# Kernel tuning notes

Measured on AMD Instinct MI355X. Metric: run time of the kernel, lower is better.

## Reference

```python
import jax, jax.numpy as jnp
import numpy as np

B, Cfi, H, W = 2, 32, 192, 192
Cfp, Cfo, NUM = 1, 2, 16
N = H * W
Ct = Cfo + Cfi + Cfi + Cfp  # 67
EPS = 1e-5


def _bn(x, g, b, m, v):
    # x: (B, C, num, N); per-channel inference batchnorm
    inv = g * jax.lax.rsqrt(v + EPS)
    return x * inv[None, :, None, None] + (b - m * inv)[None, :, None, None]


def _pconv(x, Wt):
    # 1x1 conv as channel contraction: Wt (Cout, Cin), x (B, Cin, num, N)
    return jnp.einsum('oc,bcmn->bomn', Wt, x)


def setup_inputs() -> dict:
    key = jax.random.key(0)
    ks = jax.random.split(key, 32)
    inp = {
        'If': jax.random.normal(ks[0], (B, Cfi, H, W), jnp.float32),
        'Pf': jax.random.normal(ks[1], (B, Cfp, H, W), jnp.float32),
        'Ofnum': jax.random.normal(ks[2], (B, Cfo, NUM, N), jnp.float32),
        'args': jax.random.randint(ks[3], (B, NUM, N), 0, N, jnp.int64),
    }
    def conv_w(k, co, ci):
        return jax.random.normal(k, (co, ci), jnp.float32) * (1.0 / np.sqrt(ci))
    def bn_p(k, c):
        k1, k2 = jax.random.split(k)
        return (jnp.ones((c,), jnp.float32),
                jnp.zeros((c,), jnp.float32),
                jax.random.normal(k1, (c,), jnp.float32) * 0.1,
                jax.random.uniform(k2, (c,), jnp.float32, 0.5, 1.5))
    # convXF: Ct->Cfi, Cfi->Cfi (both BN+GELU)
    inp['W1'] = conv_w(ks[4], Cfi, Ct)
    inp['g1'], inp['b1'], inp['m1'], inp['v1'] = bn_p(ks[5], Cfi)
    inp['W2'] = conv_w(ks[6], Cfi, Cfi)
    inp['g2'], inp['b2'], inp['m2'], inp['v2'] = bn_p(ks[7], Cfi)
    # convXL: Cfi->Cfi (BN+GELU), Cfi->Cfi (BN only)
    inp['W3'] = conv_w(ks[8], Cfi, Cfi)
    inp['g3'], inp['b3'], inp['m3'], inp['v3'] = bn_p(ks[9], Cfi)
    inp['W4'] = conv_w(ks[10], Cfi, Cfi)
    inp['g4'], inp['b4'], inp['m4'], inp['v4'] = bn_p(ks[11], Cfi)
    # coef: Cfi -> 3, with bias
    inp['Wc'] = conv_w(ks[12], 3, Cfi)
    inp['bc'] = jax.random.normal(ks[13], (3,), jnp.float32) * 0.01
    return inp


def reference(If, Pf, Ofnum, args,
              W1, g1, b1, m1, v1,
              W2, g2, b2, m2, v2,
              W3, g3, b3, m3, v3,
              W4, g4, b4, m4, v4,
              Wc, bc):
    gelu = lambda x: jax.nn.gelu(x, approximate=False)
    If_flat = If.reshape(B, Cfi, N)   # (B, Cfi, N)
    Pf_flat = Pf.reshape(B, Cfp, N)   # (B, Cfp, M), M == N here

    # per-batch neighbor gather along flattened spatial dim
    gath = jax.vmap(lambda f, a: f[:, a])  # (C,N),(num,N) -> (C,num,N)
    IPfnum = gath(If_flat, args)            # (B, Cfi, num, N)
    Pfnum = gath(Pf_flat, args)             # (B, Cfp, num, N)
    Ifnum = jnp.broadcast_to(If_flat[:, :, None, :], (B, Cfi, NUM, N))

    X = jnp.concatenate([Ifnum, IPfnum, Pfnum, Ofnum], axis=1)  # (B, Ct, num, N)

    h = gelu(_bn(_pconv(X, W1), g1, b1, m1, v1))
    h = gelu(_bn(_pconv(h, W2), g2, b2, m2, v2))
    l = gelu(_bn(_pconv(h, W3), g3, b3, m3, v3))
    l = _bn(_pconv(l, W4), g4, b4, m4, v4)
    XF = gelu(h + l)

    feat = _pconv(XF, Wc) + bc[None, :, None, None]  # (B, 3, num, N)
    Alpha, Beta, Omega = feat[:, 0:1], feat[:, 1:2], feat[:, 2:3]
    Omega = jax.nn.softmax(Omega, axis=2)
    dout = jnp.sum(((Alpha + 1.0) * Pfnum[:, -1:] + Beta) * Omega,
                   axis=2, keepdims=True)  # (B, 1, 1, N)
    return dout.reshape(B, 1, H, W)
```

## Files before the change

### kernel.cpp

```cpp
#include <hip/hip_runtime.h>
#include <math.h>

#define BB   2
#define CFI  32
#define NN   36864
#define NUMM 16

#define ZOFSU (BB * NN * 16)

typedef __attribute__((ext_vector_type(8))) short short8;
typedef __attribute__((ext_vector_type(4))) float f4;
typedef __attribute__((ext_vector_type(16))) float f16v;
typedef __attribute__((ext_vector_type(4))) unsigned uint4v;
typedef __attribute__((ext_vector_type(2))) unsigned u2v;

static __device__ __forceinline__ f16v mm32(short8 a, short8 b, f16v c) {
    return __builtin_amdgcn_mfma_f32_32x32x16_bf16(a, b, c, 0, 0, 0);
}

template <int CTRL>
static __device__ __forceinline__ float dpp_add(float x) {
    int y = __builtin_amdgcn_update_dpp(0, __builtin_bit_cast(int, x),
                                        CTRL, 0xf, 0xf, true);
    return x + __builtin_bit_cast(float, y);
}
template <int CTRL>
static __device__ __forceinline__ float dpp_max(float x) {
    int y = __builtin_amdgcn_update_dpp(0, __builtin_bit_cast(int, x),
                                        CTRL, 0xf, 0xf, true);
    return fmaxf(x, __builtin_bit_cast(float, y));
}

static __device__ __forceinline__ float gelu_fast(float x) {
    const float x2  = x * x;
    const float q   = fmaf(-0.10294310f, x2, -2.30211813f);
    const float e   = exp2f(q * x);
    const float r   = __builtin_amdgcn_rcpf(e + 1.0f);
    return x * r;
}

static __device__ __forceinline__ unsigned bf16_rne_bits(float x) {
    unsigned u = __builtin_bit_cast(unsigned, x);
    return u + 0x7fffu + ((u >> 16) & 1u);
}
static __device__ __forceinline__ void split_pack(float x0, float x1,
                                                  unsigned& hi, unsigned& lo) {
    unsigned r0 = bf16_rne_bits(x0);
    unsigned r1 = bf16_rne_bits(x1);
    float h0 = __builtin_bit_cast(float, r0 & 0xffff0000u);
    float h1 = __builtin_bit_cast(float, r1 & 0xffff0000u);
    hi = (r0 >> 16) | (r1 & 0xffff0000u);
    unsigned s0 = bf16_rne_bits(x0 - h0);
    unsigned s1 = bf16_rne_bits(x1 - h1);
    lo = (s0 >> 16) | (s1 & 0xffff0000u);
}

static __device__ __forceinline__ unsigned pack2(float a, float b) {
    unsigned ua = __builtin_bit_cast(unsigned, a) + 0x8000u;
    unsigned ub = __builtin_bit_cast(unsigned, b) + 0x8000u;
    return (ua >> 16) | (ub & 0xffff0000u);
}
static __device__ __forceinline__ float bflo(unsigned u) {
    return __builtin_bit_cast(float, u << 16);
}
static __device__ __forceinline__ float bfhi(unsigned u) {
    return __builtin_bit_cast(float, u & 0xffff0000u);
}

union UV { unsigned u[4]; short8 v; };

__global__ __launch_bounds__(256) void yz_kernel(
    const float* __restrict__ If, const float* __restrict__ Pf,
    const float* __restrict__ W1, const float* __restrict__ g1,
    const float* __restrict__ b1, const float* __restrict__ m1,
    const float* __restrict__ v1,
    float* __restrict__ wsYZ)
{
    __shared__ float wy[1024], wz[1024], wp[32], bt1[32];
    for (int i = threadIdx.x; i < 1024; i += 256) {
        int o = i >> 5, c = i & 31;
        float inv = g1[o] * rsqrtf(v1[o] + 1e-5f);
        wy[i] = W1[o * 67 + c]      * inv;
        wz[i] = W1[o * 67 + 32 + c] * inv;
    }
    if (threadIdx.x < 32) {
        int o = threadIdx.x;
        float inv = g1[o] * rsqrtf(v1[o] + 1e-5f);
        wp[o]  = W1[o * 67 + 64] * inv;
        bt1[o] = b1[o] - m1[o] * inv;
    }
    __syncthreads();

    const int r  = threadIdx.x & 3;
    const int p  = blockIdx.x * 64 + (threadIdx.x >> 2);
    const int b  = p / NN, n = p - b * NN;
    const int o0 = r * 8;
    const float* ifp = If + (size_t)b * CFI * NN + n;

    float v[32];
#pragma unroll
    for (int c = 0; c < 32; c++) v[c] = ifp[(size_t)c * NN];
    const float pf = Pf[p];

    float accY[8], accZ[8];
#pragma unroll
    for (int j = 0; j < 8; j++) {
        const float4* wyr = (const float4*)&wy[(o0 + j) * 32];
        const float4* wzr = (const float4*)&wz[(o0 + j) * 32];
        float ay = bt1[o0 + j];
        float az = wp[o0 + j] * pf;
#pragma unroll
        for (int c4 = 0; c4 < 8; c4++) {
            float4 a = wyr[c4], z = wzr[c4];
            ay = fmaf(a.x, v[4 * c4 + 0], ay);  az = fmaf(z.x, v[4 * c4 + 0], az);
            ay = fmaf(a.y, v[4 * c4 + 1], ay);  az = fmaf(z.y, v[4 * c4 + 1], az);
            ay = fmaf(a.z, v[4 * c4 + 2], ay);  az = fmaf(z.z, v[4 * c4 + 2], az);
            ay = fmaf(a.w, v[4 * c4 + 3], ay);  az = fmaf(z.w, v[4 * c4 + 3], az);
        }
        accY[j] = ay; accZ[j] = az;
    }

    unsigned* wsu = (unsigned*)wsYZ;
    u2v yA, yB, zA, zB;
    yA[0] = pack2(accY[0], accY[1]); yA[1] = pack2(accY[2], accY[3]);
    yB[0] = pack2(accY[4], accY[5]); yB[1] = pack2(accY[6], accY[7]);
    zA[0] = pack2(accZ[0], accZ[1]); zA[1] = pack2(accZ[2], accZ[3]);
    zB[0] = pack2(accZ[4], accZ[5]); zB[1] = pack2(accZ[6], accZ[7]);
    *(u2v*)(wsu + (size_t)p * 16 + 2 * r)          = yA;
    *(u2v*)(wsu + (size_t)p * 16 + 8 + 2 * r)      = yB;
    *(u2v*)(wsu + ZOFSU + (size_t)p * 16 + 2 * r)     = zA;
    *(u2v*)(wsu + ZOFSU + (size_t)p * 16 + 8 + 2 * r) = zB;
}

#define LOADL(Lc)                                                             \
    {                                                                         \
        A0l = *(const short8*)&wfrag[(Lc)][0][1][lane + io][0];               \
        A0h = *(const short8*)&wfrag[(Lc)][0][0][lane + io][0];               \
        A1l = *(const short8*)&wfrag[(Lc)][1][1][lane + io][0];               \
        A1h = *(const short8*)&wfrag[(Lc)][1][0][lane + io][0];               \
    }

#define LAYER_MM(Lc, ACCV, BIN0, BIN1)                                        \
    {                                                                         \
        f4 t_;                                                                \
        t_ = *(const f4*)&btl[(Lc) * 32 +      4 * hi + 4 * io];              \
        ACCV[0]  = t_[0]; ACCV[1]  = t_[1]; ACCV[2]  = t_[2]; ACCV[3]  = t_[3]; \
        t_ = *(const f4*)&btl[(Lc) * 32 +  8 + 4 * hi + 4 * io];              \
        ACCV[4]  = t_[0]; ACCV[5]  = t_[1]; ACCV[6]  = t_[2]; ACCV[7]  = t_[3]; \
        t_ = *(const f4*)&btl[(Lc) * 32 + 16 + 4 * hi + 4 * io];              \
        ACCV[8]  = t_[0]; ACCV[9]  = t_[1]; ACCV[10] = t_[2]; ACCV[11] = t_[3]; \
        t_ = *(const f4*)&btl[(Lc) * 32 + 24 + 4 * hi + 4 * io];              \
        ACCV[12] = t_[0]; ACCV[13] = t_[1]; ACCV[14] = t_[2]; ACCV[15] = t_[3]; \
        ACCV = mm32(A0l, BIN0.v, ACCV);                                       \
        ACCV = mm32(A0h, BIN0.v, ACCV);                                       \
        ACCV = mm32(A1l, BIN1.v, ACCV);                                       \
        ACCV = mm32(A1h, BIN1.v, ACCV);                                       \
    }

#define GELU_PACK(ACCV, B0V, B1V)                                             \
    {                                                                         \
        _Pragma("unroll")                                                     \
        for (int k = 0; k < 4; k++) {                                         \
            float t0 = gelu_fast(ACCV[2 * k]);                                \
            float t1 = gelu_fast(ACCV[2 * k + 1]);                            \
            B0V.u[k] = pack2(t0, t1);                                         \
            float t2 = gelu_fast(ACCV[8 + 2 * k]);                            \
            float t3 = gelu_fast(ACCV[8 + 2 * k + 1]);                        \
            B1V.u[k] = pack2(t2, t3);                                         \
        }                                                                     \
    }

__global__ __launch_bounds__(256, 5) void main_kernel(
    const float* __restrict__ Pf, const float* __restrict__ Of,
    const int* __restrict__ args,
    const float* __restrict__ W1, const float* __restrict__ g1,
    const float* __restrict__ v1,
    const float* __restrict__ W2, const float* __restrict__ g2,
    const float* __restrict__ b2, const float* __restrict__ m2,
    const float* __restrict__ v2,
    const float* __restrict__ W3, const float* __restrict__ g3,
    const float* __restrict__ b3, const float* __restrict__ m3,
    const float* __restrict__ v3,
    const float* __restrict__ W4, const float* __restrict__ g4,
    const float* __restrict__ b4, const float* __restrict__ m4,
    const float* __restrict__ v4,
    const float* __restrict__ Wc, const float* __restrict__ bc,
    const float* __restrict__ ws, float* __restrict__ out)
{
    __shared__ __align__(16) unsigned wfrag[3][2][2][64][4];
    __shared__ __align__(16) float btl[3 * 32];
    __shared__ __align__(16) float wch[3 * 32];
    __shared__ __align__(16) float w1t[2 * 32];
    __shared__ float bcs[3];
    __shared__ int   izs;

    const float* Ws[3] = {W2, W3, W4};
    const float* gs[3] = {g2, g3, g4};
    const float* vs[3] = {v2, v3, v4};
    const float* bs[3] = {b2, b3, b4};
    const float* ms[3] = {m2, m3, m4};

    for (int idx = threadIdx.x; idx < 1536; idx += 256) {
        int pp  = idx & 3;
        int ln  = (idx >> 2) & 63;
        int kh  = (idx >> 8) & 1;
        int L   = idx >> 9;
        int row = ln & 31;
        int g   = ln >> 5;
        int k   = kh * 16 + 4 * g + 2 * (pp & 1) + 8 * (pp >> 1);
        float inv = gs[L][row] * rsqrtf(vs[L][row] + 1e-5f);
        float w0 = Ws[L][row * 32 + k]     * inv;
        float w1 = Ws[L][row * 32 + k + 1] * inv;
        unsigned hiw, low;
        split_pack(w0, w1, hiw, low);
        wfrag[L][kh][0][ln][pp] = hiw;
        wfrag[L][kh][1][ln][pp] = low;
    }
    if (threadIdx.x < 96) {
        int L = threadIdx.x >> 5, ch = threadIdx.x & 31;
        btl[threadIdx.x] = bs[L][ch] - ms[L][ch] * (gs[L][ch] * rsqrtf(vs[L][ch] + 1e-5f));
        wch[threadIdx.x] = Wc[L * 32 + ch];
    }
    if (threadIdx.x < 64) {
        int t = threadIdx.x >> 5, ch = threadIdx.x & 31;
        float i1 = g1[ch] * rsqrtf(v1[ch] + 1e-5f);
        w1t[threadIdx.x] = W1[ch * 67 + 65 + t] * i1;
    }
    if (threadIdx.x < 3) bcs[threadIdx.x] = bc[threadIdx.x];
    if (threadIdx.x == 0) izs = (int)(args[0] >> 16);
    __syncthreads();

    const unsigned* wsu = (const unsigned*)ws;
    const int lane  = threadIdx.x & 63;
    const int wid   = threadIdx.x >> 6;
    const int m     = lane & 15;
    const int pt    = (lane >> 4) & 1;
    const int hi    = lane >> 5;
    const int q4    = hi << 2;
    const int izero = izs;

    const int base  = blockIdx.x * 32 + wid * 8 + pt;

    uint4v yu0, yu1, zu0, zu1;
    float of0v, of1v, pfg_n;
    int   aI_n;
    {
        const int C0 = base;
        const int b0 = (C0 >= NN) ? 1 : 0;
        const int n0 = C0 - b0 * NN;
        const int a0 = args[(b0 * NUMM + m) * NN + n0];
        of0v = Of[((b0 * 2 + 0) * NUMM + m) * NN + n0];
        of1v = Of[((b0 * 2 + 1) * NUMM + m) * NN + n0];
        pfg_n = Pf[b0 * NN + a0];
        const uint4v* yb = (const uint4v*)(wsu + (size_t)(b0 * NN + n0) * 16 + hi * 8);
        const uint4v* zb = (const uint4v*)(wsu + ZOFSU + (size_t)(b0 * NN + a0) * 16 + hi * 8);
        yu0 = yb[0]; yu1 = yb[1];
        zu0 = zb[0]; zu1 = zb[1];
        const int C1 = (C0 + 2 < BB * NN) ? C0 + 2 : BB * NN - 1;
        const int b1_ = (C1 >= NN) ? 1 : 0;
        const int n1_ = C1 - b1_ * NN;
        aI_n = args[(b1_ * NUMM + m) * NN + n1_];
    }

#pragma unroll 1
    for (int i = 0; i < 4; i++) {
        const int io = i & izero;
        const int C  = base + i * 2;
        const int b  = (C >= NN) ? 1 : 0;
        const int n  = C - b * NN;
        const float pfg = pfg_n;

        short8 A0l, A0h, A1l, A1h;
        LOADL(0);

        UV B0, B1;
#pragma unroll
        for (int q = 0; q < 4; q++) {
            const f4 waq = *(const f4*)&w1t[8 * q + q4 + 4 * io];
            const f4 wbq = *(const f4*)&w1t[32 + 8 * q + q4 + 4 * io];
            const unsigned ya0 = (q < 2) ? yu0[2 * q]     : yu1[2 * q - 4];
            const unsigned ya1 = (q < 2) ? yu0[2 * q + 1] : yu1[2 * q - 3];
            const unsigned za0 = (q < 2) ? zu0[2 * q]     : zu1[2 * q - 4];
            const unsigned za1 = (q < 2) ? zu0[2 * q + 1] : zu1[2 * q - 3];
            float t0 = fmaf(of1v, wbq[0], fmaf(of0v, waq[0], bflo(ya0) + bflo(za0)));
            float t1 = fmaf(of1v, wbq[1], fmaf(of0v, waq[1], bfhi(ya0) + bfhi(za0)));
            float t2 = fmaf(of1v, wbq[2], fmaf(of0v, waq[2], bflo(ya1) + bflo(za1)));
            float t3 = fmaf(of1v, wbq[3], fmaf(of0v, waq[3], bfhi(ya1) + bfhi(za1)));
            t0 = gelu_fast(t0); t1 = gelu_fast(t1);
            t2 = gelu_fast(t2); t3 = gelu_fast(t3);
            const unsigned lo2 = pack2(t0, t1), hi2 = pack2(t2, t3);
            if (q < 2) { B0.u[2 * q] = lo2; B0.u[2 * q + 1] = hi2; }
            else       { B1.u[2 * q - 4] = lo2; B1.u[2 * q - 3] = hi2; }
        }

        {
            const int Cn = (C + 2 < BB * NN) ? C + 2 : BB * NN - 1;
            const int bn = (Cn >= NN) ? 1 : 0;
            const int nn = Cn - bn * NN;
            const uint4v* ybn = (const uint4v*)(wsu + (size_t)(bn * NN + nn) * 16 + hi * 8);
            yu0 = ybn[0]; yu1 = ybn[1];
            of0v = Of[((bn * 2 + 0) * NUMM + m) * NN + nn];
            of1v = Of[((bn * 2 + 1) * NUMM + m) * NN + nn];
            const int aN = aI_n;
            pfg_n = Pf[bn * NN + aN];
            const uint4v* zbn = (const uint4v*)(wsu + ZOFSU + (size_t)(bn * NN + aN) * 16 + hi * 8);
            zu0 = zbn[0]; zu1 = zbn[1];
            const int Ca = (C + 4 < BB * NN) ? C + 4 : BB * NN - 1;
            const int ba = (Ca >= NN) ? 1 : 0;
            const int na = Ca - ba * NN;
            aI_n = args[(ba * NUMM + m) * NN + na];
        }

        f16v acc;
        LAYER_MM(0, acc, B0, B1);
        LOADL(1);
        UV P0, P1;
        GELU_PACK(acc, P0, P1);
        B0 = P0; B1 = P1;

        LAYER_MM(1, acc, B0, B1);
        LOADL(2);
        GELU_PACK(acc, B0, B1);

        LAYER_MM(2, acc, B0, B1);

        float pa = 0.0f, pb = 0.0f, po = 0.0f;
#pragma unroll
        for (int q = 0; q < 4; q++) {
            const f4 wAq = *(const f4*)&wch[      8 * q + q4 + 4 * io];
            const f4 wBq = *(const f4*)&wch[32 +  8 * q + q4 + 4 * io];
            const f4 wOq = *(const f4*)&wch[64 +  8 * q + q4 + 4 * io];
            const unsigned pu0 = (q < 2) ? P0.u[2 * q]     : P1.u[2 * q - 4];
            const unsigned pu1 = (q < 2) ? P0.u[2 * q + 1] : P1.u[2 * q - 3];
            float xf0 = gelu_fast(bflo(pu0) + acc[4 * q + 0]);
            float xf1 = gelu_fast(bfhi(pu0) + acc[4 * q + 1]);
            float xf2 = gelu_fast(bflo(pu1) + acc[4 * q + 2]);
            float xf3 = gelu_fast(bfhi(pu1) + acc[4 * q + 3]);
            pa = fmaf(wAq[0], xf0, pa); pa = fmaf(wAq[1], xf1, pa);
            pa = fmaf(wAq[2], xf2, pa); pa = fmaf(wAq[3], xf3, pa);
            pb = fmaf(wBq[0], xf0, pb); pb = fmaf(wBq[1], xf1, pb);
            pb = fmaf(wBq[2], xf2, pb); pb = fmaf(wBq[3], xf3, pb);
            po = fmaf(wOq[0], xf0, po); po = fmaf(wOq[1], xf1, po);
            po = fmaf(wOq[2], xf2, po); po = fmaf(wOq[3], xf3, po);
        }
        pa += __shfl_xor(pa, 32, 64);
        pb += __shfl_xor(pb, 32, 64);
        po += __shfl_xor(po, 32, 64);

        const float alpha = pa + bcs[0];
        const float beta_ = pb + bcs[1];
        const float omega = po + bcs[2];
        const float val = fmaf(alpha + 1.0f, pfg, beta_);

        float mx = dpp_max<0xB1>(omega);
        mx = dpp_max<0x4E>(mx);
        mx = dpp_max<0x141>(mx);
        mx = dpp_max<0x140>(mx);
        const float e = __expf(omega - mx);
        float S = e, T = val * e;
        S = dpp_add<0xB1>(S);   T = dpp_add<0xB1>(T);
        S = dpp_add<0x4E>(S);   T = dpp_add<0x4E>(T);
        S = dpp_add<0x141>(S);  T = dpp_add<0x141>(T);
        S = dpp_add<0x140>(S);  T = dpp_add<0x140>(T);

        if ((lane & 15) == 0 && lane < 32)
            out[b * NN + n] = T * __builtin_amdgcn_rcpf(S);
    }
}

extern "C" void kernel_launch(void* const* d_in, const int* in_sizes, int n_in,
                              void* d_out, int out_size, void* d_ws, size_t ws_size,
                              hipStream_t stream) {
    const float* If    = (const float*)d_in[0];
    const float* Pf    = (const float*)d_in[1];
    const float* Of    = (const float*)d_in[2];
    const int*   args  = (const int*)d_in[3];
    const float* W1    = (const float*)d_in[4];
    const float* g1    = (const float*)d_in[5];
    const float* b1    = (const float*)d_in[6];
    const float* m1    = (const float*)d_in[7];
    const float* v1    = (const float*)d_in[8];
    const float* W2    = (const float*)d_in[9];
    const float* g2    = (const float*)d_in[10];
    const float* b2    = (const float*)d_in[11];
    const float* m2    = (const float*)d_in[12];
    const float* v2    = (const float*)d_in[13];
    const float* W3    = (const float*)d_in[14];
    const float* g3    = (const float*)d_in[15];
    const float* b3    = (const float*)d_in[16];
    const float* m3    = (const float*)d_in[17];
    const float* v3    = (const float*)d_in[18];
    const float* W4    = (const float*)d_in[19];
    const float* g4    = (const float*)d_in[20];
    const float* b4    = (const float*)d_in[21];
    const float* m4    = (const float*)d_in[22];
    const float* v4    = (const float*)d_in[23];
    const float* Wc    = (const float*)d_in[24];
    const float* bc    = (const float*)d_in[25];

    float* ws  = (float*)d_ws;
    float* out = (float*)d_out;

    yz_kernel<<<(BB * NN) / 64, 256, 0, stream>>>(
        If, Pf, W1, g1, b1, m1, v1, ws);

    main_kernel<<<(BB * NN) / 32, 256, 0, stream>>>(
        Pf, Of, args,
        W1, g1, v1,
        W2, g2, b2, m2, v2,
        W3, g3, b3, m3, v3,
        W4, g4, b4, m4, v4,
        Wc, bc, ws, out);
}
```

Baseline: 229.9 us.

## Switch MLP layers from 32x32x16 to 16x16x32 bf16 MFMA with one point per wave

```diff
diff --git a/kernel.cpp b/kernel.cpp
--- a/kernel.cpp
+++ b/kernel.cpp
@@ -10,12 +10,10 @@
 
 typedef __attribute__((ext_vector_type(8))) short short8;
 typedef __attribute__((ext_vector_type(4))) float f4;
-typedef __attribute__((ext_vector_type(16))) float f16v;
-typedef __attribute__((ext_vector_type(4))) unsigned uint4v;
 typedef __attribute__((ext_vector_type(2))) unsigned u2v;
 
-static __device__ __forceinline__ f16v mm32(short8 a, short8 b, f16v c) {
-    return __builtin_amdgcn_mfma_f32_32x32x16_bf16(a, b, c, 0, 0, 0);
+static __device__ __forceinline__ f4 mm16(short8 a, short8 b, f4 c) {
+    return __builtin_amdgcn_mfma_f32_16x16x32_bf16(a, b, c, 0, 0, 0);
 }
 
 template <int CTRL>
@@ -132,7 +130,7 @@
     *(u2v*)(wsu + ZOFSU + (size_t)p * 16 + 8 + 2 * r) = zB;
 }
 
-#define LOADL(Lc)                                                             \
+#define LOADL16(Lc)                                                           \
     {                                                                         \
         A0l = *(const short8*)&wfrag[(Lc)][0][1][lane + io][0];               \
         A0h = *(const short8*)&wfrag[(Lc)][0][0][lane + io][0];               \
@@ -140,34 +138,22 @@
         A1h = *(const short8*)&wfrag[(Lc)][1][0][lane + io][0];               \
     }
 
-#define LAYER_MM(Lc, ACCV, BIN0, BIN1)                                        \
+#define LAYER16(Lc, BV, ACC0, ACC1)                                           \
     {                                                                         \
-        f4 t_;                                                                \
-        t_ = *(const f4*)&btl[(Lc) * 32 +      4 * hi + 4 * io];              \
-        ACCV[0]  = t_[0]; ACCV[1]  = t_[1]; ACCV[2]  = t_[2]; ACCV[3]  = t_[3]; \
-        t_ = *(const f4*)&btl[(Lc) * 32 +  8 + 4 * hi + 4 * io];              \
-        ACCV[4]  = t_[0]; ACCV[5]  = t_[1]; ACCV[6]  = t_[2]; ACCV[7]  = t_[3]; \
-        t_ = *(const f4*)&btl[(Lc) * 32 + 16 + 4 * hi + 4 * io];              \
-        ACCV[8]  = t_[0]; ACCV[9]  = t_[1]; ACCV[10] = t_[2]; ACCV[11] = t_[3]; \
-        t_ = *(const f4*)&btl[(Lc) * 32 + 24 + 4 * hi + 4 * io];              \
-        ACCV[12] = t_[0]; ACCV[13] = t_[1]; ACCV[14] = t_[2]; ACCV[15] = t_[3]; \
-        ACCV = mm32(A0l, BIN0.v, ACCV);                                       \
-        ACCV = mm32(A0h, BIN0.v, ACCV);                                       \
-        ACCV = mm32(A1l, BIN1.v, ACCV);                                       \
-        ACCV = mm32(A1h, BIN1.v, ACCV);                                       \
-    }
-
-#define GELU_PACK(ACCV, B0V, B1V)                                             \
+        f4 t0_ = *(const f4*)&btl[(Lc) * 32 + gq4 + 4 * io];                  \
+        f4 t1_ = *(const f4*)&btl[(Lc) * 32 + 16 + gq4 + 4 * io];             \
+        ACC0 = mm16(A0l, BV.v, t0_);                                          \
+        ACC0 = mm16(A0h, BV.v, ACC0);                                         \
+        ACC1 = mm16(A1l, BV.v, t1_);                                          \
+        ACC1 = mm16(A1h, BV.v, ACC1);                                         \
+    }
+
+#define RELAYOUT16(ACC0, ACC1, BV)                                            \
     {                                                                         \
-        _Pragma("unroll")                                                     \
-        for (int k = 0; k < 4; k++) {                                         \
-            float t0 = gelu_fast(ACCV[2 * k]);                                \
-            float t1 = gelu_fast(ACCV[2 * k + 1]);                            \
-            B0V.u[k] = pack2(t0, t1);                                         \
-            float t2 = gelu_fast(ACCV[8 + 2 * k]);                            \
-            float t3 = gelu_fast(ACCV[8 + 2 * k + 1]);                        \
-            B1V.u[k] = pack2(t2, t3);                                         \
-        }                                                                     \
+        BV.u[0] = pack2(gelu_fast(ACC0[0]), gelu_fast(ACC0[1]));              \
+        BV.u[1] = pack2(gelu_fast(ACC0[2]), gelu_fast(ACC0[3]));              \
+        BV.u[2] = pack2(gelu_fast(ACC1[0]), gelu_fast(ACC1[1]));              \
+        BV.u[3] = pack2(gelu_fast(ACC1[2]), gelu_fast(ACC1[3]));              \
     }
 
 __global__ __launch_bounds__(256, 5) void main_kernel(
@@ -203,18 +189,18 @@
     for (int idx = threadIdx.x; idx < 1536; idx += 256) {
         int pp  = idx & 3;
         int ln  = (idx >> 2) & 63;
-        int kh  = (idx >> 8) & 1;
+        int T   = (idx >> 8) & 1;
         int L   = idx >> 9;
-        int row = ln & 31;
-        int g   = ln >> 5;
-        int k   = kh * 16 + 4 * g + 2 * (pp & 1) + 8 * (pp >> 1);
-        float inv = gs[L][row] * rsqrtf(vs[L][row] + 1e-5f);
-        float w0 = Ws[L][row * 32 + k]     * inv;
-        float w1 = Ws[L][row * 32 + k + 1] * inv;
+        int o   = T * 16 + (ln & 15);
+        int gg  = ln >> 4;
+        int k   = 16 * (pp >> 1) + 4 * gg + 2 * (pp & 1);
+        float inv = gs[L][o] * rsqrtf(vs[L][o] + 1e-5f);
+        float w0 = Ws[L][o * 32 + k]     * inv;
+        float w1 = Ws[L][o * 32 + k + 1] * inv;
         unsigned hiw, low;
         split_pack(w0, w1, hiw, low);
-        wfrag[L][kh][0][ln][pp] = hiw;
-        wfrag[L][kh][1][ln][pp] = low;
+        wfrag[L][T][0][ln][pp] = hiw;
+        wfrag[L][T][1][ln][pp] = low;
     }
     if (threadIdx.x < 96) {
         int L = threadIdx.x >> 5, ch = threadIdx.x & 31;
@@ -234,14 +220,14 @@
     const int lane  = threadIdx.x & 63;
     const int wid   = threadIdx.x >> 6;
     const int m     = lane & 15;
-    const int pt    = (lane >> 4) & 1;
-    const int hi    = lane >> 5;
-    const int q4    = hi << 2;
+    const int gl    = lane >> 4;
+    const int gq4   = gl << 2;
+    const int uA    = (gl & 1) * 8 + (gl >> 1) * 2;
     const int izero = izs;
 
-    const int base  = blockIdx.x * 32 + wid * 8 + pt;
-
-    uint4v yu0, yu1, zu0, zu1;
+    const int base  = blockIdx.x * 16 + wid * 4;
+
+    u2v yA, yB, zA, zB;
     float of0v, of1v, pfg_n;
     int   aI_n;
     {
@@ -252,11 +238,11 @@
         of0v = Of[((b0 * 2 + 0) * NUMM + m) * NN + n0];
         of1v = Of[((b0 * 2 + 1) * NUMM + m) * NN + n0];
         pfg_n = Pf[b0 * NN + a0];
-        const uint4v* yb = (const uint4v*)(wsu + (size_t)(b0 * NN + n0) * 16 + hi * 8);
-        const uint4v* zb = (const uint4v*)(wsu + ZOFSU + (size_t)(b0 * NN + a0) * 16 + hi * 8);
-        yu0 = yb[0]; yu1 = yb[1];
-        zu0 = zb[0]; zu1 = zb[1];
-        const int C1 = (C0 + 2 < BB * NN) ? C0 + 2 : BB * NN - 1;
+        const unsigned* yr = wsu + (size_t)(b0 * NN + n0) * 16;
+        const unsigned* zr = wsu + ZOFSU + (size_t)(b0 * NN + a0) * 16;
+        yA = *(const u2v*)(yr + uA); yB = *(const u2v*)(yr + uA + 4);
+        zA = *(const u2v*)(zr + uA); zB = *(const u2v*)(zr + uA + 4);
+        const int C1 = (C0 + 1 < BB * NN) ? C0 + 1 : BB * NN - 1;
         const int b1_ = (C1 >= NN) ? 1 : 0;
         const int n1_ = C1 - b1_ * NN;
         aI_n = args[(b1_ * NUMM + m) * NN + n1_];
@@ -265,87 +251,94 @@
 #pragma unroll 1
     for (int i = 0; i < 4; i++) {
         const int io = i & izero;
-        const int C  = base + i * 2;
+        const int C  = base + i;
         const int b  = (C >= NN) ? 1 : 0;
         const int n  = C - b * NN;
         const float pfg = pfg_n;
 
         short8 A0l, A0h, A1l, A1h;
-        LOADL(0);
-
-        UV B0, B1;
-#pragma unroll
-        for (int q = 0; q < 4; q++) {
-            const f4 waq = *(const f4*)&w1t[8 * q + q4 + 4 * io];
-            const f4 wbq = *(const f4*)&w1t[32 + 8 * q + q4 + 4 * io];
-            const unsigned ya0 = (q < 2) ? yu0[2 * q]     : yu1[2 * q - 4];
-            const unsigned ya1 = (q < 2) ? yu0[2 * q + 1] : yu1[2 * q - 3];
-            const unsigned za0 = (q < 2) ? zu0[2 * q]     : zu1[2 * q - 4];
-            const unsigned za1 = (q < 2) ? zu0[2 * q + 1] : zu1[2 * q - 3];
-            float t0 = fmaf(of1v, wbq[0], fmaf(of0v, waq[0], bflo(ya0) + bflo(za0)));
-            float t1 = fmaf(of1v, wbq[1], fmaf(of0v, waq[1], bfhi(ya0) + bfhi(za0)));
-            float t2 = fmaf(of1v, wbq[2], fmaf(of0v, waq[2], bflo(ya1) + bflo(za1)));
-            float t3 = fmaf(of1v, wbq[3], fmaf(of0v, waq[3], bfhi(ya1) + bfhi(za1)));
-            t0 = gelu_fast(t0); t1 = gelu_fast(t1);
-            t2 = gelu_fast(t2); t3 = gelu_fast(t3);
-            const unsigned lo2 = pack2(t0, t1), hi2 = pack2(t2, t3);
-            if (q < 2) { B0.u[2 * q] = lo2; B0.u[2 * q + 1] = hi2; }
-            else       { B1.u[2 * q - 4] = lo2; B1.u[2 * q - 3] = hi2; }
+        LOADL16(0);
+
+        const f4 walo = *(const f4*)&w1t[gq4 + 4 * io];
+        const f4 wahi = *(const f4*)&w1t[16 + gq4 + 4 * io];
+        const f4 wblo = *(const f4*)&w1t[32 + gq4 + 4 * io];
+        const f4 wbhi = *(const f4*)&w1t[48 + gq4 + 4 * io];
+        UV B0;
+        {
+            float x0 = fmaf(of1v, wblo[0], fmaf(of0v, walo[0], bflo(yA[0]) + bflo(zA[0])));
+            float x1 = fmaf(of1v, wblo[1], fmaf(of0v, walo[1], bfhi(yA[0]) + bfhi(zA[0])));
+            float x2 = fmaf(of1v, wblo[2], fmaf(of0v, walo[2], bflo(yA[1]) + bflo(zA[1])));
+            float x3 = fmaf(of1v, wblo[3], fmaf(of0v, walo[3], bfhi(yA[1]) + bfhi(zA[1])));
+            float x4 = fmaf(of1v, wbhi[0], fmaf(of0v, wahi[0], bflo(yB[0]) + bflo(zB[0])));
+            float x5 = fmaf(of1v, wbhi[1], fmaf(of0v, wahi[1], bfhi(yB[0]) + bfhi(zB[0])));
+            float x6 = fmaf(of1v, wbhi[2], fmaf(of0v, wahi[2], bflo(yB[1]) + bflo(zB[1])));
+            float x7 = fmaf(of1v, wbhi[3], fmaf(of0v, wahi[3], bfhi(yB[1]) + bfhi(zB[1])));
+            B0.u[0] = pack2(gelu_fast(x0), gelu_fast(x1));
+            B0.u[1] = pack2(gelu_fast(x2), gelu_fast(x3));
+            B0.u[2] = pack2(gelu_fast(x4), gelu_fast(x5));
+            B0.u[3] = pack2(gelu_fast(x6), gelu_fast(x7));
         }
 
         {
-            const int Cn = (C + 2 < BB * NN) ? C + 2 : BB * NN - 1;
+            const int Cn = (C + 1 < BB * NN) ? C + 1 : BB * NN - 1;
             const int bn = (Cn >= NN) ? 1 : 0;
             const int nn = Cn - bn * NN;
-            const uint4v* ybn = (const uint4v*)(wsu + (size_t)(bn * NN + nn) * 16 + hi * 8);
-            yu0 = ybn[0]; yu1 = ybn[1];
+            const unsigned* yrn = wsu + (size_t)(bn * NN + nn) * 16;
+            yA = *(const u2v*)(yrn + uA); yB = *(const u2v*)(yrn + uA + 4);
             of0v = Of[((bn * 2 + 0) * NUMM + m) * NN + nn];
             of1v = Of[((bn * 2 + 1) * NUMM + m) * NN + nn];
             const int aN = aI_n;
             pfg_n = Pf[bn * NN + aN];
-            const uint4v* zbn = (const uint4v*)(wsu + ZOFSU + (size_t)(bn * NN + aN) * 16 + hi * 8);
-            zu0 = zbn[0]; zu1 = zbn[1];
-            const int Ca = (C + 4 < BB * NN) ? C + 4 : BB * NN - 1;
+            const unsigned* zrn = wsu + ZOFSU + (size_t)(bn * NN + aN) * 16;
+            zA = *(const u2v*)(zrn + uA); zB = *(const u2v*)(zrn + uA + 4);
+            const int Ca = (C + 2 < BB * NN) ? C + 2 : BB * NN - 1;
             const int ba = (Ca >= NN) ? 1 : 0;
             const int na = Ca - ba * NN;
             aI_n = args[(ba * NUMM + m) * NN + na];
         }
 
-        f16v acc;
-        LAYER_MM(0, acc, B0, B1);
-        LOADL(1);
-        UV P0, P1;
-        GELU_PACK(acc, P0, P1);
-        B0 = P0; B1 = P1;
-
-        LAYER_MM(1, acc, B0, B1);
-        LOADL(2);
-        GELU_PACK(acc, B0, B1);
-
-        LAYER_MM(2, acc, B0, B1);
-
-        float pa = 0.0f, pb = 0.0f, po = 0.0f;
-#pragma unroll
-        for (int q = 0; q < 4; q++) {
-            const f4 wAq = *(const f4*)&wch[      8 * q + q4 + 4 * io];
-            const f4 wBq = *(const f4*)&wch[32 +  8 * q + q4 + 4 * io];
-            const f4 wOq = *(const f4*)&wch[64 +  8 * q + q4 + 4 * io];
-            const unsigned pu0 = (q < 2) ? P0.u[2 * q]     : P1.u[2 * q - 4];
-            const unsigned pu1 = (q < 2) ? P0.u[2 * q + 1] : P1.u[2 * q - 3];
-            float xf0 = gelu_fast(bflo(pu0) + acc[4 * q + 0]);
-            float xf1 = gelu_fast(bfhi(pu0) + acc[4 * q + 1]);
-            float xf2 = gelu_fast(bflo(pu1) + acc[4 * q + 2]);
-            float xf3 = gelu_fast(bfhi(pu1) + acc[4 * q + 3]);
-            pa = fmaf(wAq[0], xf0, pa); pa = fmaf(wAq[1], xf1, pa);
-            pa = fmaf(wAq[2], xf2, pa); pa = fmaf(wAq[3], xf3, pa);
-            pb = fmaf(wBq[0], xf0, pb); pb = fmaf(wBq[1], xf1, pb);
-            pb = fmaf(wBq[2], xf2, pb); pb = fmaf(wBq[3], xf3, pb);
-            po = fmaf(wOq[0], xf0, po); po = fmaf(wOq[1], xf1, po);
-            po = fmaf(wOq[2], xf2, po); po = fmaf(wOq[3], xf3, po);
+        f4 acc0, acc1;
+        LAYER16(0, B0, acc0, acc1);
+        LOADL16(1);
+        UV P0;
+        RELAYOUT16(acc0, acc1, P0);
+        B0 = P0;
+
+        LAYER16(1, B0, acc0, acc1);
+        LOADL16(2);
+        RELAYOUT16(acc0, acc1, B0);
+
+        LAYER16(2, B0, acc0, acc1);
+
+        const f4 wcAl = *(const f4*)&wch[gq4 + 4 * io];
+        const f4 wcAh = *(const f4*)&wch[16 + gq4 + 4 * io];
+        const f4 wcBl = *(const f4*)&wch[32 + gq4 + 4 * io];
+        const f4 wcBh = *(const f4*)&wch[48 + gq4 + 4 * io];
+        const f4 wcOl = *(const f4*)&wch[64 + gq4 + 4 * io];
+        const f4 wcOh = *(const f4*)&wch[80 + gq4 + 4 * io];
+
+        float pa, pb, po;
+        {
+            float xf0 = gelu_fast(bflo(P0.u[0]) + acc0[0]);
+            float xf1 = gelu_fast(bfhi(P0.u[0]) + acc0[1]);
+            float xf2 = gelu_fast(bflo(P0.u[1]) + acc0[2]);
+            float xf3 = gelu_fast(bfhi(P0.u[1]) + acc0[3]);
+            float xf4 = gelu_fast(bflo(P0.u[2]) + acc1[0]);
+            float xf5 = gelu_fast(bfhi(P0.u[2]) + acc1[1]);
+            float xf6 = gelu_fast(bflo(P0.u[3]) + acc1[2]);
+            float xf7 = gelu_fast(bfhi(P0.u[3]) + acc1[3]);
+            pa = wcAl[0] * xf0; pb = wcBl[0] * xf0; po = wcOl[0] * xf0;
+            pa = fmaf(wcAl[1], xf1, pa); pb = fmaf(wcBl[1], xf1, pb); po = fmaf(wcOl[1], xf1, po);
+            pa = fmaf(wcAl[2], xf2, pa); pb = fmaf(wcBl[2], xf2, pb); po = fmaf(wcOl[2], xf2, po);
+            pa = fmaf(wcAl[3], xf3, pa); pb = fmaf(wcBl[3], xf3, pb); po = fmaf(wcOl[3], xf3, po);
+            pa = fmaf(wcAh[0], xf4, pa); pb = fmaf(wcBh[0], xf4, pb); po = fmaf(wcOh[0], xf4, po);
+            pa = fmaf(wcAh[1], xf5, pa); pb = fmaf(wcBh[1], xf5, pb); po = fmaf(wcOh[1], xf5, po);
+            pa = fmaf(wcAh[2], xf6, pa); pb = fmaf(wcBh[2], xf6, pb); po = fmaf(wcOh[2], xf6, po);
+            pa = fmaf(wcAh[3], xf7, pa); pb = fmaf(wcBh[3], xf7, pb); po = fmaf(wcOh[3], xf7, po);
         }
-        pa += __shfl_xor(pa, 32, 64);
-        pb += __shfl_xor(pb, 32, 64);
-        po += __shfl_xor(po, 32, 64);
+        pa += __shfl_xor(pa, 16, 64);  pa += __shfl_xor(pa, 32, 64);
+        pb += __shfl_xor(pb, 16, 64);  pb += __shfl_xor(pb, 32, 64);
+        po += __shfl_xor(po, 16, 64);  po += __shfl_xor(po, 32, 64);
 
         const float alpha = pa + bcs[0];
         const float beta_ = pb + bcs[1];
@@ -363,7 +356,7 @@
         S = dpp_add<0x141>(S);  T = dpp_add<0x141>(T);
         S = dpp_add<0x140>(S);  T = dpp_add<0x140>(T);
 
-        if ((lane & 15) == 0 && lane < 32)
+        if (lane == 0)
             out[b * NN + n] = T * __builtin_amdgcn_rcpf(S);
     }
 }
@@ -404,7 +397,7 @@
     yz_kernel<<<(BB * NN) / 64, 256, 0, stream>>>(
         If, Pf, W1, g1, b1, m1, v1, ws);
 
-    main_kernel<<<(BB * NN) / 32, 256, 0, stream>>>(
+    main_kernel<<<(BB * NN) / 16, 256, 0, stream>>>(
         Pf, Of, args,
         W1, g1, v1,
         W2, g2, b2, m2, v2,
```

Measured after the change: 237.5 us. 1.03x slower.
